# Optimization experiments

Hardware: AMD Instinct MI355X
Metric: run time of the kernel (lower is better)

The kernel has to match this reference:

```python
import jax, jax.numpy as jnp
import numpy as np

B, S, E = 8, 1025, 768
H, D = 12, 64  # num_heads, head_dim


def setup_inputs() -> dict:
    key = jax.random.key(0)
    ks = jax.random.split(key, 11)
    sc = 1.0 / np.sqrt(E)
    def lin(k):
        kw, kb = jax.random.split(k)
        return (jax.random.normal(kw, (E, E), jnp.float32) * sc,
                jax.random.normal(kb, (E,), jnp.float32) * sc)
    Wq, bq = lin(ks[0]); Wk, bk = lin(ks[1]); Wv, bv = lin(ks[2])
    Wc, bc = lin(ks[3]); Wo, bo = lin(ks[4])
    x = jax.random.normal(ks[5], (B, S, E), jnp.float32)
    return {"x": x, "Wq": Wq, "bq": bq, "Wk": Wk, "bk": bk,
            "Wv": Wv, "bv": bv, "Wc": Wc, "bc": bc, "Wo": Wo, "bo": bo}


def _heads(y, b, n):
    # [b, n, E] -> [b, H, n, D]
    return y.reshape(b, n, H, D).transpose(0, 2, 1, 3)


def reference(x, Wq, bq, Wk, bk, Wv, bv, Wc, bc, Wo, bo):
    b, s, e = x.shape
    n = s - 1  # special_cls strips the CLS token
    cls_token = x[:, 0, :]            # [b, E]
    xt = x[:, 1:, :]                  # [b, n, E]

    q = _heads(xt @ Wq.T + bq, b, n)  # [b, H, n, D]
    k = _heads(xt @ Wk.T + bk, b, n)
    v = _heads(xt @ Wv.T + bv, b, n)

    qk_dot = jnp.einsum('bhqd,bhkd->bhqk', q, k)             # [b,H,n,n]
    q_norm2 = jnp.clip((q ** 2).sum(-1, keepdims=True), 1e-5)  # [b,H,n,1]

    c = (cls_token @ Wc.T + bc).reshape(b, 1, H, D).transpose(0, 2, 1, 3)  # [b,H,1,D]
    cq_dot = jnp.einsum('bhod,bhqd->bhoq', c, q)             # [b,H,1,n]
    c_norm2 = jnp.clip((c ** 2).sum(-1, keepdims=True), 1e-5)  # [b,H,1,1]

    attn_logits = qk_dot * cq_dot.transpose(0, 1, 3, 2) / (q_norm2 * jnp.sqrt(D * c_norm2))

    ck_dot = jnp.einsum('bhod,bhkd->bhok', c, k)             # [b,H,1,n]
    attn_logits_for_cls = ck_dot / jnp.sqrt(D * c_norm2)
    cls_out = jnp.einsum('bhok,bhkd->bhod', attn_logits_for_cls, v).reshape(b, 1, H * D)

    attn = jax.nn.softmax(attn_logits, axis=-1)              # [b,H,n,n]
    values = jnp.einsum('bhqk,bhkd->bhqd', attn, v)          # [b,H,n,D]

    cls_out = (cls_token[:, None, :] + cls_out) * 0.5        # [b,1,E]
    values = jnp.concatenate(
        [cls_out, values.transpose(0, 2, 1, 3).reshape(b, n, e)], axis=1)  # [b,S,E]
    out = values @ Wo.T + bo
    return out, attn
```

## Files before the change

### kernel.cpp

```cpp
#include <hip/hip_runtime.h>

#define B_ 8
#define S_ 1025
#define E_ 768
#define H_ 12
#define D_ 64
#define N_ 1024
#define M_OUT (B_*S_)

typedef _Float16 half8_t __attribute__((ext_vector_type(8)));
typedef _Float16 half4_t __attribute__((ext_vector_type(4)));
typedef short short8_t __attribute__((ext_vector_type(8)));
typedef float f32x4 __attribute__((ext_vector_type(4)));

#define MFMA_F16(A, B, C)  __builtin_amdgcn_mfma_f32_16x16x32_f16((A), (B), (C), 0, 0, 0)
#define MFMA_BF16(A, B, C) __builtin_amdgcn_mfma_f32_16x16x32_bf16((A), (B), (C), 0, 0, 0)

__device__ __forceinline__ unsigned short f2bf(float f) {
  unsigned u = __float_as_uint(f);
  u += 0x7FFFu + ((u >> 16) & 1u);
  return (unsigned short)(u >> 16);
}
__device__ __forceinline__ float bf2f(unsigned short s) {
  return __uint_as_float(((unsigned)s) << 16);
}

__global__ __launch_bounds__(256) void split_x_kernel(
    const float* __restrict__ x, _Float16* __restrict__ xh, _Float16* __restrict__ xl)
{
  const int idx = blockIdx.x * 256 + threadIdx.x;
  const int row = idx / 192;
  const int c   = (idx % 192) * 4;
  const int xrow = row + (row >> 10) + 1;
  float4 v = *(const float4*)&x[(long)xrow*E_ + c];
  float f[4] = {v.x, v.y, v.z, v.w};
  half4_t hs, ls;
  #pragma unroll
  for (int t = 0; t < 4; ++t) {
    _Float16 hh = (_Float16)f[t];
    hs[t] = hh; ls[t] = (_Float16)(f[t] - (float)hh);
  }
  *(half4_t*)&xh[(long)row*E_ + c] = hs;
  *(half4_t*)&xl[(long)row*E_ + c] = ls;
}

__global__ __launch_bounds__(256) void split_w_kernel(
    const float* __restrict__ W0, const float* __restrict__ W1,
    const float* __restrict__ W2, const float* __restrict__ W3,
    _Float16* __restrict__ h0, _Float16* __restrict__ l0,
    _Float16* __restrict__ h1, _Float16* __restrict__ l1,
    _Float16* __restrict__ h2, _Float16* __restrict__ l2,
    _Float16* __restrict__ h3, _Float16* __restrict__ l3)
{
  const int which = blockIdx.y;
  const float* __restrict__ W = (which==0)?W0:(which==1)?W1:(which==2)?W2:W3;
  _Float16* __restrict__ oh   = (which==0)?h0:(which==1)?h1:(which==2)?h2:h3;
  _Float16* __restrict__ ol   = (which==0)?l0:(which==1)?l1:(which==2)?l2:l3;
  const int idx = blockIdx.x * 256 + threadIdx.x;
  const long off = (long)idx * 4;
  float4 v = *(const float4*)&W[off];
  float f[4] = {v.x, v.y, v.z, v.w};
  half4_t hs, ls;
  #pragma unroll
  for (int t = 0; t < 4; ++t) {
    _Float16 hh = (_Float16)f[t];
    hs[t] = hh; ls[t] = (_Float16)(f[t] - (float)hh);
  }
  *(half4_t*)&oh[off] = hs;
  *(half4_t*)&ol[off] = ls;
}

__global__ __launch_bounds__(256) void proj_qkv_kernel(
    const _Float16* __restrict__ xh, const _Float16* __restrict__ xl,
    const _Float16* __restrict__ wqh, const _Float16* __restrict__ wql,
    const _Float16* __restrict__ wkh, const _Float16* __restrict__ wkl,
    const _Float16* __restrict__ wvh, const _Float16* __restrict__ wvl,
    const float* __restrict__ bq, const float* __restrict__ bk, const float* __restrict__ bv,
    _Float16* __restrict__ qh, _Float16* __restrict__ ql,
    _Float16* __restrict__ kh, _Float16* __restrict__ kl,
    unsigned short* __restrict__ vth, unsigned short* __restrict__ vtl)
{
  __shared__ _Float16 Ah[128][40];
  __shared__ _Float16 Al[128][40];
  __shared__ _Float16 Bh[128][40];
  __shared__ _Float16 Bl[128][40];

  const int which = blockIdx.z;
  const _Float16* __restrict__ wh = (which==0)?wqh:(which==1)?wkh:wvh;
  const _Float16* __restrict__ wl = (which==0)?wql:(which==1)?wkl:wvl;
  const float* __restrict__ bias  = (which==0)?bq:(which==1)?bk:bv;

  const int tid  = threadIdx.x;
  const int lane = tid & 63;
  const int wv   = tid >> 6;
  const int wm   = wv >> 1, wn = wv & 1;
  const int m0   = blockIdx.y * 128;
  const int n0   = blockIdx.x * 128;

  const int srow = tid >> 1;
  const int scol = (tid & 1) << 4;

  const long arow = (long)(m0 + srow) * E_ + scol;
  const long brow = (long)(n0 + srow) * E_ + scol;

  f32x4 acc[4][4] = {};

  const int fr = lane & 15;
  const int kb = (lane >> 4) << 3;
  const int ar0 = wm * 64 + fr;
  const int br0 = wn * 64 + fr;

  for (int k0 = 0; k0 < E_; k0 += 32) {
    half8_t a_h0 = *(const half8_t*)&xh[arow + k0];
    half8_t a_h1 = *(const half8_t*)&xh[arow + k0 + 8];
    half8_t a_l0 = *(const half8_t*)&xl[arow + k0];
    half8_t a_l1 = *(const half8_t*)&xl[arow + k0 + 8];
    half8_t b_h0 = *(const half8_t*)&wh[brow + k0];
    half8_t b_h1 = *(const half8_t*)&wh[brow + k0 + 8];
    half8_t b_l0 = *(const half8_t*)&wl[brow + k0];
    half8_t b_l1 = *(const half8_t*)&wl[brow + k0 + 8];
    __syncthreads();
    *(half8_t*)&Ah[srow][scol]   = a_h0;  *(half8_t*)&Ah[srow][scol+8] = a_h1;
    *(half8_t*)&Al[srow][scol]   = a_l0;  *(half8_t*)&Al[srow][scol+8] = a_l1;
    *(half8_t*)&Bh[srow][scol]   = b_h0;  *(half8_t*)&Bh[srow][scol+8] = b_h1;
    *(half8_t*)&Bl[srow][scol]   = b_l0;  *(half8_t*)&Bl[srow][scol+8] = b_l1;
    __syncthreads();

    half8_t fah[4], fal[4], fbh[4], fbl[4];
    #pragma unroll
    for (int mi = 0; mi < 4; ++mi) {
      fah[mi] = *(const half8_t*)&Ah[ar0 + mi*16][kb];
      fal[mi] = *(const half8_t*)&Al[ar0 + mi*16][kb];
    }
    #pragma unroll
    for (int ni = 0; ni < 4; ++ni) {
      fbh[ni] = *(const half8_t*)&Bh[br0 + ni*16][kb];
      fbl[ni] = *(const half8_t*)&Bl[br0 + ni*16][kb];
    }
    #pragma unroll
    for (int mi = 0; mi < 4; ++mi)
      #pragma unroll
      for (int ni = 0; ni < 4; ++ni) {
        acc[mi][ni] = MFMA_F16(fah[mi], fbh[ni], acc[mi][ni]);
        acc[mi][ni] = MFMA_F16(fal[mi], fbh[ni], acc[mi][ni]);
        acc[mi][ni] = MFMA_F16(fah[mi], fbl[ni], acc[mi][ni]);
      }
  }

  const int rr = (lane >> 4) << 2;
  if (which < 2) {
    _Float16* __restrict__ oh = (which==0) ? qh : kh;
    _Float16* __restrict__ ol = (which==0) ? ql : kl;
    #pragma unroll
    for (int ni = 0; ni < 4; ++ni) {
      const int c = n0 + wn*64 + ni*16 + fr;
      const float bb = bias[c];
      #pragma unroll
      for (int mi = 0; mi < 4; ++mi) {
        const int row0 = m0 + wm*64 + mi*16 + rr;
        #pragma unroll
        for (int j = 0; j < 4; ++j) {
          float r = acc[mi][ni][j] + bb;
          _Float16 hh = (_Float16)r;
          oh[(long)(row0+j)*E_ + c] = hh;
          ol[(long)(row0+j)*E_ + c] = (_Float16)(r - (float)hh);
        }
      }
    }
  } else {
    #pragma unroll
    for (int ni = 0; ni < 4; ++ni) {
      const int c = n0 + wn*64 + ni*16 + fr;
      const int h_ = c >> 6, d_ = c & 63;
      const float bb = bias[c];
      #pragma unroll
      for (int mi = 0; mi < 4; ++mi) {
        const int row0 = m0 + wm*64 + mi*16 + rr;
        #pragma unroll
        for (int j = 0; j < 4; ++j) {
          const int row = row0 + j;
          const int b_ = row >> 10, n_ = row & 1023;
          float r = acc[mi][ni][j] + bb;
          unsigned short hb = f2bf(r);
          const long o = ((long)(b_*H_ + h_)*64 + d_)*N_ + n_;
          vth[o] = hb;
          vtl[o] = f2bf(r - bf2f(hb));
        }
      }
    }
  }
}

__global__ __launch_bounds__(256) void proj_out_kernel(
    const _Float16* __restrict__ ah_g, const _Float16* __restrict__ al_g,
    const _Float16* __restrict__ wh, const _Float16* __restrict__ wl,
    const float* __restrict__ bias, float* __restrict__ out)
{
  __shared__ _Float16 Ah[128][40];
  __shared__ _Float16 Al[128][40];
  __shared__ _Float16 Bh[128][40];
  __shared__ _Float16 Bl[128][40];

  const int tid  = threadIdx.x;
  const int lane = tid & 63;
  const int wv   = tid >> 6;
  const int wm   = wv >> 1, wn = wv & 1;
  const int m0   = blockIdx.y * 128;
  const int n0   = blockIdx.x * 128;

  const int srow = tid >> 1;
  const int scol = (tid & 1) << 4;

  const int gm = m0 + srow;
  const bool aok = gm < M_OUT;
  const long arow = (long)gm * E_ + scol;
  const long brow = (long)(n0 + srow) * E_ + scol;

  f32x4 acc[4][4] = {};

  const int fr = lane & 15;
  const int kb = (lane >> 4) << 3;
  const int ar0 = wm * 64 + fr;
  const int br0 = wn * 64 + fr;

  for (int k0 = 0; k0 < E_; k0 += 32) {
    half8_t a_h0 = {}, a_h1 = {}, a_l0 = {}, a_l1 = {};
    if (aok) {
      a_h0 = *(const half8_t*)&ah_g[arow + k0];
      a_h1 = *(const half8_t*)&ah_g[arow + k0 + 8];
      a_l0 = *(const half8_t*)&al_g[arow + k0];
      a_l1 = *(const half8_t*)&al_g[arow + k0 + 8];
    }
    half8_t b_h0 = *(const half8_t*)&wh[brow + k0];
    half8_t b_h1 = *(const half8_t*)&wh[brow + k0 + 8];
    half8_t b_l0 = *(const half8_t*)&wl[brow + k0];
    half8_t b_l1 = *(const half8_t*)&wl[brow + k0 + 8];
    __syncthreads();
    *(half8_t*)&Ah[srow][scol]   = a_h0;  *(half8_t*)&Ah[srow][scol+8] = a_h1;
    *(half8_t*)&Al[srow][scol]   = a_l0;  *(half8_t*)&Al[srow][scol+8] = a_l1;
    *(half8_t*)&Bh[srow][scol]   = b_h0;  *(half8_t*)&Bh[srow][scol+8] = b_h1;
    *(half8_t*)&Bl[srow][scol]   = b_l0;  *(half8_t*)&Bl[srow][scol+8] = b_l1;
    __syncthreads();

    half8_t fah[4], fal[4], fbh[4], fbl[4];
    #pragma unroll
    for (int mi = 0; mi < 4; ++mi) {
      fah[mi] = *(const half8_t*)&Ah[ar0 + mi*16][kb];
      fal[mi] = *(const half8_t*)&Al[ar0 + mi*16][kb];
    }
    #pragma unroll
    for (int ni = 0; ni < 4; ++ni) {
      fbh[ni] = *(const half8_t*)&Bh[br0 + ni*16][kb];
      fbl[ni] = *(const half8_t*)&Bl[br0 + ni*16][kb];
    }
    #pragma unroll
    for (int mi = 0; mi < 4; ++mi)
      #pragma unroll
      for (int ni = 0; ni < 4; ++ni) {
        acc[mi][ni] = MFMA_F16(fah[mi], fbh[ni], acc[mi][ni]);
        acc[mi][ni] = MFMA_F16(fal[mi], fbh[ni], acc[mi][ni]);
        acc[mi][ni] = MFMA_F16(fah[mi], fbl[ni], acc[mi][ni]);
      }
  }

  const int rr = (lane >> 4) << 2;
  #pragma unroll
  for (int ni = 0; ni < 4; ++ni) {
    const int c = n0 + wn*64 + ni*16 + fr;
    const float bb = bias[c];
    #pragma unroll
    for (int mi = 0; mi < 4; ++mi) {
      const int row = m0 + wm*64 + mi*16 + rr;
      #pragma unroll
      for (int j = 0; j < 4; ++j) {
        if (row + j < M_OUT)
          out[(long)(row + j) * E_ + c] = acc[mi][ni][j] + bb;
      }
    }
  }
}

__global__ __launch_bounds__(64) void cls_c_kernel(
    const float* __restrict__ x, const float* __restrict__ Wc, const float* __restrict__ bc,
    float* __restrict__ cbuf, float* __restrict__ cdenom)
{
  const int bh = blockIdx.x;
  const int b = bh / H_, h = bh % H_;
  const int d = threadIdx.x;
  const float* xr = x + (long)b*S_*E_;
  const float* wr = Wc + (long)(h*D_ + d)*E_;
  float acc = 0.f;
  for (int j = 0; j < E_; j += 4) {
    float4 xw = *(const float4*)&xr[j];
    float4 ww = *(const float4*)&wr[j];
    acc += xw.x*ww.x + xw.y*ww.y + xw.z*ww.z + xw.w*ww.w;
  }
  acc += bc[h*D_ + d];
  cbuf[bh*D_ + d] = acc;
  float sq = acc*acc;
  #pragma unroll
  for (int off = 32; off > 0; off >>= 1) sq += __shfl_xor(sq, off);
  if (d == 0) cdenom[bh] = rsqrtf((float)D_ * fmaxf(sq, 1e-5f));
}

__global__ __launch_bounds__(256) void attn_kernel(
    const _Float16* __restrict__ qh, const _Float16* __restrict__ ql,
    const _Float16* __restrict__ kh, const _Float16* __restrict__ kl,
    const unsigned short* __restrict__ vth, const unsigned short* __restrict__ vtl,
    const float* __restrict__ cbuf, const float* __restrict__ cdenom,
    _Float16* __restrict__ valsh, _Float16* __restrict__ vall,
    float* __restrict__ rowl_g, float* __restrict__ attn)
{
  __shared__ short QPh[64][72];
  __shared__ short QPl[64][72];
  __shared__ short Kh_s[64][72];
  __shared__ short Kl_s[64][72];
  __shared__ short Vth_s[64][72];
  __shared__ short Vtl_s[64][72];
  __shared__ float cs[64];
  __shared__ float rowscale_s[64];
  __shared__ float rowsum2[2][64];

  const int qt = blockIdx.x, h = blockIdx.y, b = blockIdx.z;
  const int bh = b * H_ + h;
  const int q0 = qt * 64;
  const int tid  = threadIdx.x;
  const int lane = tid & 63;
  const int wv   = tid >> 6;
  const int wm   = wv >> 1, wn = wv & 1;
  const int fr   = lane & 15;
  const int g    = lane >> 4;
  const int lr   = tid >> 2;
  const int lc   = (tid & 3) * 16;

  {
    const long qbase = ((long)b*N_ + q0 + lr)*E_ + h*D_ + lc;
    *(half8_t*)&QPh[lr][lc]   = *(const half8_t*)&qh[qbase];
    *(half8_t*)&QPh[lr][lc+8] = *(const half8_t*)&qh[qbase+8];
    *(half8_t*)&QPl[lr][lc]   = *(const half8_t*)&ql[qbase];
    *(half8_t*)&QPl[lr][lc+8] = *(const half8_t*)&ql[qbase+8];
  }
  if (tid < 64) cs[tid] = cbuf[bh*D_ + tid];
  const float cdn = cdenom[bh];
  __syncthreads();

  if (tid < 64) {
    const _Float16* qhr = (const _Float16*)QPh[tid];
    const _Float16* qlr = (const _Float16*)QPl[tid];
    float qn2 = 0.f, cq = 0.f;
    #pragma unroll 8
    for (int d = 0; d < 64; ++d) {
      float qv = (float)qhr[d] + (float)qlr[d];
      qn2 = fmaf(qv, qv, qn2);
      cq  = fmaf(cs[d], qv, cq);
    }
    rowscale_s[tid] = cq * cdn / fmaxf(qn2, 1e-5f);
  }

  half8_t qfh[2][2], qfl[2][2];
  #pragma unroll
  for (int mi = 0; mi < 2; ++mi)
    #pragma unroll
    for (int ks = 0; ks < 2; ++ks) {
      qfh[mi][ks] = *(const half8_t*)&QPh[wm*32 + mi*16 + fr][ks*32 + g*8];
      qfl[mi][ks] = *(const half8_t*)&QPl[wm*32 + mi*16 + fr][ks*32 + g*8];
    }
  __syncthreads();

  float rs[2][4];
  #pragma unroll
  for (int mi = 0; mi < 2; ++mi)
    #pragma unroll
    for (int j = 0; j < 4; ++j)
      rs[mi][j] = rowscale_s[wm*32 + mi*16 + g*4 + j];

  float psum[2][4] = {};
  f32x4 acc[2][2] = {};

  for (int kt = 0; kt < 16; ++kt) {
    __syncthreads();
    {
      const long kbase = ((long)b*N_ + kt*64 + lr)*E_ + h*D_ + lc;
      *(half8_t*)&Kh_s[lr][lc]   = *(const half8_t*)&kh[kbase];
      *(half8_t*)&Kh_s[lr][lc+8] = *(const half8_t*)&kh[kbase+8];
      *(half8_t*)&Kl_s[lr][lc]   = *(const half8_t*)&kl[kbase];
      *(half8_t*)&Kl_s[lr][lc+8] = *(const half8_t*)&kl[kbase+8];
    }
    {
      const long vbase = ((long)bh*64 + lr)*N_ + kt*64 + lc;
      *(short8_t*)&Vth_s[lr][lc]   = *(const short8_t*)(vth + vbase);
      *(short8_t*)&Vth_s[lr][lc+8] = *(const short8_t*)(vth + vbase + 8);
      *(short8_t*)&Vtl_s[lr][lc]   = *(const short8_t*)(vtl + vbase);
      *(short8_t*)&Vtl_s[lr][lc+8] = *(const short8_t*)(vtl + vbase + 8);
    }
    __syncthreads();

    f32x4 sacc[2][2] = {};
    #pragma unroll
    for (int ks = 0; ks < 2; ++ks) {
      half8_t kfh[2], kfl[2];
      #pragma unroll
      for (int ni = 0; ni < 2; ++ni) {
        kfh[ni] = *(const half8_t*)&Kh_s[wn*32 + ni*16 + fr][ks*32 + g*8];
        kfl[ni] = *(const half8_t*)&Kl_s[wn*32 + ni*16 + fr][ks*32 + g*8];
      }
      #pragma unroll
      for (int mi = 0; mi < 2; ++mi)
        #pragma unroll
        for (int ni = 0; ni < 2; ++ni) {
          sacc[mi][ni] = MFMA_F16(qfh[mi][ks], kfh[ni], sacc[mi][ni]);
          sacc[mi][ni] = MFMA_F16(qfl[mi][ks], kfh[ni], sacc[mi][ni]);
          sacc[mi][ni] = MFMA_F16(qfh[mi][ks], kfl[ni], sacc[mi][ni]);
        }
    }

    #pragma unroll
    for (int mi = 0; mi < 2; ++mi)
      #pragma unroll
      for (int ni = 0; ni < 2; ++ni)
        #pragma unroll
        for (int j = 0; j < 4; ++j) {
          const int row = wm*32 + mi*16 + g*4 + j;
          const int col = wn*32 + ni*16 + fr;
          float s = sacc[mi][ni][j] * rs[mi][j];
          float p = __expf(fminf(s, 60.f));
          psum[mi][j] += p;
          attn[((long)(bh*N_ + q0 + row) << 10) + kt*64 + col] = p;
          unsigned short hb = f2bf(p);
          QPh[row][col] = (short)hb;
          QPl[row][col] = (short)f2bf(p - bf2f(hb));
        }
    __syncthreads();

    #pragma unroll
    for (int ks = 0; ks < 2; ++ks) {
      short8_t pfh[2], pfl[2], vfh[2], vfl[2];
      #pragma unroll
      for (int mi = 0; mi < 2; ++mi) {
        pfh[mi] = *(const short8_t*)&QPh[wm*32 + mi*16 + fr][ks*32 + g*8];
        pfl[mi] = *(const short8_t*)&QPl[wm*32 + mi*16 + fr][ks*32 + g*8];
      }
      #pragma unroll
      for (int nj = 0; nj < 2; ++nj) {
        vfh[nj] = *(const short8_t*)&Vth_s[wn*32 + nj*16 + fr][ks*32 + g*8];
        vfl[nj] = *(const short8_t*)&Vtl_s[wn*32 + nj*16 + fr][ks*32 + g*8];
      }
      #pragma unroll
      for (int mi = 0; mi < 2; ++mi)
        #pragma unroll
        for (int nj = 0; nj < 2; ++nj) {
          acc[mi][nj] = MFMA_BF16(pfh[mi], vfh[nj], acc[mi][nj]);
          acc[mi][nj] = MFMA_BF16(pfl[mi], vfh[nj], acc[mi][nj]);
          acc[mi][nj] = MFMA_BF16(pfh[mi], vfl[nj], acc[mi][nj]);
        }
    }
  }

  #pragma unroll
  for (int mi = 0; mi < 2; ++mi)
    #pragma unroll
    for (int j = 0; j < 4; ++j) {
      float v = psum[mi][j];
      v += __shfl_xor(v, 1);
      v += __shfl_xor(v, 2);
      v += __shfl_xor(v, 4);
      v += __shfl_xor(v, 8);
      psum[mi][j] = v;
    }
  __syncthreads();
  if (fr == 0) {
    #pragma unroll
    for (int mi = 0; mi < 2; ++mi)
      #pragma unroll
      for (int j = 0; j < 4; ++j)
        rowsum2[wn][wm*32 + mi*16 + g*4 + j] = psum[mi][j];
  }
  __syncthreads();

  if (tid < 64)
    rowl_g[(long)bh*N_ + q0 + tid] = rowsum2[0][tid] + rowsum2[1][tid];

  #pragma unroll
  for (int mi = 0; mi < 2; ++mi)
    #pragma unroll
    for (int j = 0; j < 4; ++j) {
      const int row = wm*32 + mi*16 + g*4 + j;
      const float inv = 1.0f / (rowsum2[0][row] + rowsum2[1][row]);
      #pragma unroll
      for (int nj = 0; nj < 2; ++nj) {
        const int col = wn*32 + nj*16 + fr;
        const long vo = ((long)b*S_ + 1 + q0 + row)*E_ + h*D_ + col;
        float r = acc[mi][nj][j] * inv;
        _Float16 hh = (_Float16)r;
        valsh[vo] = hh;
        vall[vo]  = (_Float16)(r - (float)hh);
      }
    }
}

__global__ __launch_bounds__(256) void cls_attn_kernel(
    const float* __restrict__ x,
    const _Float16* __restrict__ kh, const _Float16* __restrict__ kl,
    const unsigned short* __restrict__ vth, const unsigned short* __restrict__ vtl,
    const float* __restrict__ cbuf, const float* __restrict__ cdenom,
    _Float16* __restrict__ valsh, _Float16* __restrict__ vall)
{
  __shared__ float cs[64];
  __shared__ float part[4][64];
  const int bh = blockIdx.x;
  const int b = bh / H_, h = bh % H_;
  const int tid = threadIdx.x;
  const int wv = tid >> 6, lane = tid & 63;
  if (tid < 64) cs[tid] = cbuf[bh*D_ + tid];
  __syncthreads();
  float acc = 0.f;
  const long kbase0 = (long)b*N_*E_ + h*D_ + lane;
  const long vtbase = ((long)bh*64 + lane)*N_;
  for (int kk = wv*256; kk < wv*256 + 256; ++kk) {
    const long kbase = kbase0 + (long)kk*E_;
    float kv = (float)kh[kbase] + (float)kl[kbase];
    float s = cs[lane] * kv;
    s += __shfl_xor(s, 1);  s += __shfl_xor(s, 2);  s += __shfl_xor(s, 4);
    s += __shfl_xor(s, 8);  s += __shfl_xor(s, 16); s += __shfl_xor(s, 32);
    float vvv = bf2f(vth[vtbase + kk]) + bf2f(vtl[vtbase + kk]);
    acc = fmaf(s, vvv, acc);
  }
  part[wv][lane] = acc;
  __syncthreads();
  if (tid < 64) {
    const float tot = (part[0][tid] + part[1][tid] + part[2][tid] + part[3][tid]) * cdenom[bh];
    const float cls = x[(long)b*S_*E_ + h*D_ + tid];
    float r = (cls + tot) * 0.5f;
    const long vo = (long)b*S_*E_ + h*D_ + tid;
    _Float16 hh = (_Float16)r;
    valsh[vo] = hh;
    vall[vo]  = (_Float16)(r - (float)hh);
  }
}

__global__ __launch_bounds__(256) void rescale_kernel(
    float* __restrict__ attn, const float* __restrict__ rowl_g)
{
  const long row = blockIdx.x;
  const float inv = 1.0f / rowl_g[row];
  float* p = attn + (row << 10) + threadIdx.x * 4;
  float4 u = *(float4*)p;
  u.x *= inv; u.y *= inv; u.z *= inv; u.w *= inv;
  *(float4*)p = u;
}

extern "C" void kernel_launch(void* const* d_in, const int* in_sizes, int n_in,
                              void* d_out, int out_size, void* d_ws, size_t ws_size,
                              hipStream_t stream) {
  (void)in_sizes; (void)n_in; (void)out_size; (void)ws_size;
  const float* x  = (const float*)d_in[0];
  const float* Wq = (const float*)d_in[1];
  const float* bq = (const float*)d_in[2];
  const float* Wk = (const float*)d_in[3];
  const float* bk = (const float*)d_in[4];
  const float* Wv = (const float*)d_in[5];
  const float* bv = (const float*)d_in[6];
  const float* Wc = (const float*)d_in[7];
  const float* bc = (const float*)d_in[8];
  const float* Wo = (const float*)d_in[9];
  const float* bo = (const float*)d_in[10];

  const long XSZ = (long)8192 * E_;
  const long WSZ = (long)E_ * E_;
  const long QSZ = (long)B_ * N_ * E_;
  const long VSZ = (long)B_ * S_ * E_;

  float* outp = (float*)d_out;
  float* attn = outp + VSZ;

  _Float16* xh  = (_Float16*)attn;
  _Float16* xl  = xh + XSZ;
  _Float16* wqh = xl + XSZ;
  _Float16* wql = wqh + WSZ;
  _Float16* wkh = wql + WSZ;
  _Float16* wkl = wkh + WSZ;
  _Float16* wvh = wkl + WSZ;
  _Float16* wvl = wvh + WSZ;

  _Float16* qh = (_Float16*)d_ws;
  _Float16* ql = qh + QSZ;
  _Float16* kh = ql + QSZ;
  _Float16* kl = kh + QSZ;
  unsigned short* vth = (unsigned short*)(kl + QSZ);
  unsigned short* vtl = vth + QSZ;
  _Float16* valsh = (_Float16*)(vtl + QSZ);
  _Float16* vall  = valsh + VSZ;
  _Float16* woh   = vall + VSZ;
  _Float16* wol   = woh + WSZ;
  float* cbuf = (float*)(wol + WSZ);
  float* cden = cbuf + B_*H_*D_;
  float* rowl = cden + B_*H_;

  split_x_kernel<<<6144, 256, 0, stream>>>(x, xh, xl);
  split_w_kernel<<<dim3(576, 4), 256, 0, stream>>>(Wq, Wk, Wv, Wo,
      wqh, wql, wkh, wkl, wvh, wvl, woh, wol);
  proj_qkv_kernel<<<dim3(6, 64, 3), 256, 0, stream>>>(xh, xl,
      wqh, wql, wkh, wkl, wvh, wvl, bq, bk, bv, qh, ql, kh, kl, vth, vtl);
  cls_c_kernel<<<B_*H_, 64, 0, stream>>>(x, Wc, bc, cbuf, cden);
  attn_kernel<<<dim3(16, H_, B_), 256, 0, stream>>>(qh, ql, kh, kl, vth, vtl,
      cbuf, cden, valsh, vall, rowl, attn);
  cls_attn_kernel<<<B_*H_, 256, 0, stream>>>(x, kh, kl, vth, vtl, cbuf, cden, valsh, vall);
  rescale_kernel<<<B_*H_*N_, 256, 0, stream>>>(attn, rowl);
  proj_out_kernel<<<dim3(6, 65), 256, 0, stream>>>(valsh, vall, woh, wol, bo, outp);
}
```

Baseline: 1.037 ms.

## Fuse attention normalization into a recompute pass and stage V transpose through LDS

The attention kernel no longer writes unnormalized probabilities and then rescales them in a separate kernel. After computing row sums, it recomputes QK^T over all key tiles and writes the normalized probabilities once, which removes a full read-modify-write pass over the large attn tensor and drops the rescale launch at the cost of extra MFMA and exp work. The V projection epilogue now transposes through swizzled shared memory so it can write vectorized, coalesced rows instead of scattered 2-byte stores. The values buffer is kept in fp32, and the fp16 hi/lo split moves into the output projection's load path.

```diff
diff --git a/kernel.cpp b/kernel.cpp
--- a/kernel.cpp
+++ b/kernel.cpp
@@ -80,10 +80,11 @@
     _Float16* __restrict__ kh, _Float16* __restrict__ kl,
     unsigned short* __restrict__ vth, unsigned short* __restrict__ vtl)
 {
-  __shared__ _Float16 Ah[128][40];
-  __shared__ _Float16 Al[128][40];
-  __shared__ _Float16 Bh[128][40];
-  __shared__ _Float16 Bl[128][40];
+  __shared__ __align__(16) unsigned char smem_raw[40960];
+  _Float16 (* const Ah)[40] = (_Float16 (*)[40])(smem_raw);
+  _Float16 (* const Al)[40] = (_Float16 (*)[40])(smem_raw + 10240);
+  _Float16 (* const Bh)[40] = (_Float16 (*)[40])(smem_raw + 20480);
+  _Float16 (* const Bl)[40] = (_Float16 (*)[40])(smem_raw + 30720);
 
   const int which = blockIdx.z;
   const _Float16* __restrict__ wh = (which==0)?wqh:(which==1)?wkh:wvh;
@@ -168,31 +169,44 @@
       }
     }
   } else {
-    #pragma unroll
-    for (int ni = 0; ni < 4; ++ni) {
-      const int c = n0 + wn*64 + ni*16 + fr;
-      const int h_ = c >> 6, d_ = c & 63;
-      const float bb = bias[c];
-      #pragma unroll
-      for (int mi = 0; mi < 4; ++mi) {
-        const int row0 = m0 + wm*64 + mi*16 + rr;
+    __syncthreads();
+    short (* const Vt)[136] = (short (*)[136])(smem_raw);
+    const int b_     = m0 >> 10;
+    const int n_base = m0 & 1023;
+    const int crow = tid >> 1, hf = tid & 1;
+    const int cg   = n0 + crow;
+    const long obase = ((long)(b_*H_ + (cg >> 6))*64 + (cg & 63))*N_ + n_base + hf*64;
+    const int rswz = (crow & 7) << 3;
+    #pragma unroll
+    for (int plane = 0; plane < 2; ++plane) {
+      #pragma unroll
+      for (int ni = 0; ni < 4; ++ni) {
+        const int cl = wn*64 + ni*16 + fr;
+        const float bb = bias[n0 + cl];
         #pragma unroll
-        for (int j = 0; j < 4; ++j) {
-          const int row = row0 + j;
-          const int b_ = row >> 10, n_ = row & 1023;
-          float r = acc[mi][ni][j] + bb;
-          unsigned short hb = f2bf(r);
-          const long o = ((long)(b_*H_ + h_)*64 + d_)*N_ + n_;
-          vth[o] = hb;
-          vtl[o] = f2bf(r - bf2f(hb));
-        }
-      }
+        for (int mi = 0; mi < 4; ++mi)
+          #pragma unroll
+          for (int j = 0; j < 4; ++j) {
+            const int rl = wm*64 + mi*16 + rr + j;
+            float r = acc[mi][ni][j] + bb;
+            unsigned short hb = f2bf(r);
+            unsigned short val = plane ? f2bf(r - bf2f(hb)) : hb;
+            Vt[cl][rl ^ ((cl & 7) << 3)] = (short)val;
+          }
+      }
+      __syncthreads();
+      unsigned short* __restrict__ dst = plane ? vtl : vth;
+      #pragma unroll
+      for (int t = 0; t < 8; ++t)
+        *(short8_t*)&dst[obase + t*8] =
+            *(const short8_t*)&Vt[crow][(hf*64 + t*8) ^ rswz];
+      __syncthreads();
     }
   }
 }
 
 __global__ __launch_bounds__(256) void proj_out_kernel(
-    const _Float16* __restrict__ ah_g, const _Float16* __restrict__ al_g,
+    const float* __restrict__ A,
     const _Float16* __restrict__ wh, const _Float16* __restrict__ wl,
     const float* __restrict__ bias, float* __restrict__ out)
 {
@@ -224,20 +238,31 @@
   const int br0 = wn * 64 + fr;
 
   for (int k0 = 0; k0 < E_; k0 += 32) {
-    half8_t a_h0 = {}, a_h1 = {}, a_l0 = {}, a_l1 = {};
+    float4 a0 = make_float4(0.f,0.f,0.f,0.f), a1 = a0, a2 = a0, a3 = a0;
     if (aok) {
-      a_h0 = *(const half8_t*)&ah_g[arow + k0];
-      a_h1 = *(const half8_t*)&ah_g[arow + k0 + 8];
-      a_l0 = *(const half8_t*)&al_g[arow + k0];
-      a_l1 = *(const half8_t*)&al_g[arow + k0 + 8];
+      a0 = *(const float4*)&A[arow + k0];
+      a1 = *(const float4*)&A[arow + k0 + 4];
+      a2 = *(const float4*)&A[arow + k0 + 8];
+      a3 = *(const float4*)&A[arow + k0 + 12];
     }
     half8_t b_h0 = *(const half8_t*)&wh[brow + k0];
     half8_t b_h1 = *(const half8_t*)&wh[brow + k0 + 8];
     half8_t b_l0 = *(const half8_t*)&wl[brow + k0];
     half8_t b_l1 = *(const half8_t*)&wl[brow + k0 + 8];
     __syncthreads();
-    *(half8_t*)&Ah[srow][scol]   = a_h0;  *(half8_t*)&Ah[srow][scol+8] = a_h1;
-    *(half8_t*)&Al[srow][scol]   = a_l0;  *(half8_t*)&Al[srow][scol+8] = a_l1;
+    {
+      float av[16] = {a0.x,a0.y,a0.z,a0.w,a1.x,a1.y,a1.z,a1.w,
+                      a2.x,a2.y,a2.z,a2.w,a3.x,a3.y,a3.z,a3.w};
+      half8_t ah0, ah1, alo0, alo1;
+      #pragma unroll
+      for (int t = 0; t < 8; ++t) {
+        _Float16 hh;
+        hh = (_Float16)av[t];   ah0[t] = hh; alo0[t] = (_Float16)(av[t]   - (float)hh);
+        hh = (_Float16)av[t+8]; ah1[t] = hh; alo1[t] = (_Float16)(av[t+8] - (float)hh);
+      }
+      *(half8_t*)&Ah[srow][scol]   = ah0;  *(half8_t*)&Ah[srow][scol+8] = ah1;
+      *(half8_t*)&Al[srow][scol]   = alo0; *(half8_t*)&Al[srow][scol+8] = alo1;
+    }
     *(half8_t*)&Bh[srow][scol]   = b_h0;  *(half8_t*)&Bh[srow][scol+8] = b_h1;
     *(half8_t*)&Bl[srow][scol]   = b_l0;  *(half8_t*)&Bl[srow][scol+8] = b_l1;
     __syncthreads();
@@ -308,8 +333,7 @@
     const _Float16* __restrict__ kh, const _Float16* __restrict__ kl,
     const unsigned short* __restrict__ vth, const unsigned short* __restrict__ vtl,
     const float* __restrict__ cbuf, const float* __restrict__ cdenom,
-    _Float16* __restrict__ valsh, _Float16* __restrict__ vall,
-    float* __restrict__ rowl_g, float* __restrict__ attn)
+    float* __restrict__ vals, float* __restrict__ attn)
 {
   __shared__ short QPh[64][72];
   __shared__ short QPl[64][72];
@@ -425,7 +449,6 @@
           float s = sacc[mi][ni][j] * rs[mi][j];
           float p = __expf(fminf(s, 60.f));
           psum[mi][j] += p;
-          attn[((long)(bh*N_ + q0 + row) << 10) + kt*64 + col] = p;
           unsigned short hb = f2bf(p);
           QPh[row][col] = (short)hb;
           QPl[row][col] = (short)f2bf(p - bf2f(hb));
@@ -477,25 +500,70 @@
   }
   __syncthreads();
 
-  if (tid < 64)
-    rowl_g[(long)bh*N_ + q0 + tid] = rowsum2[0][tid] + rowsum2[1][tid];
-
+  float invr[2][4];
   #pragma unroll
   for (int mi = 0; mi < 2; ++mi)
     #pragma unroll
     for (int j = 0; j < 4; ++j) {
       const int row = wm*32 + mi*16 + g*4 + j;
-      const float inv = 1.0f / (rowsum2[0][row] + rowsum2[1][row]);
+      invr[mi][j] = 1.0f / (rowsum2[0][row] + rowsum2[1][row]);
+    }
+
+  #pragma unroll
+  for (int mi = 0; mi < 2; ++mi)
+    #pragma unroll
+    for (int j = 0; j < 4; ++j) {
+      const int row = wm*32 + mi*16 + g*4 + j;
       #pragma unroll
       for (int nj = 0; nj < 2; ++nj) {
         const int col = wn*32 + nj*16 + fr;
-        const long vo = ((long)b*S_ + 1 + q0 + row)*E_ + h*D_ + col;
-        float r = acc[mi][nj][j] * inv;
-        _Float16 hh = (_Float16)r;
-        valsh[vo] = hh;
-        vall[vo]  = (_Float16)(r - (float)hh);
-      }
-    }
+        vals[((long)b*S_ + 1 + q0 + row)*E_ + h*D_ + col] = acc[mi][nj][j] * invr[mi][j];
+      }
+    }
+
+  for (int kt = 0; kt < 16; ++kt) {
+    __syncthreads();
+    {
+      const long kbase = ((long)b*N_ + kt*64 + lr)*E_ + h*D_ + lc;
+      *(half8_t*)&Kh_s[lr][lc]   = *(const half8_t*)&kh[kbase];
+      *(half8_t*)&Kh_s[lr][lc+8] = *(const half8_t*)&kh[kbase+8];
+      *(half8_t*)&Kl_s[lr][lc]   = *(const half8_t*)&kl[kbase];
+      *(half8_t*)&Kl_s[lr][lc+8] = *(const half8_t*)&kl[kbase+8];
+    }
+    __syncthreads();
+
+    f32x4 sacc[2][2] = {};
+    #pragma unroll
+    for (int ks = 0; ks < 2; ++ks) {
+      half8_t kfh[2], kfl[2];
+      #pragma unroll
+      for (int ni = 0; ni < 2; ++ni) {
+        kfh[ni] = *(const half8_t*)&Kh_s[wn*32 + ni*16 + fr][ks*32 + g*8];
+        kfl[ni] = *(const half8_t*)&Kl_s[wn*32 + ni*16 + fr][ks*32 + g*8];
+      }
+      #pragma unroll
+      for (int mi = 0; mi < 2; ++mi)
+        #pragma unroll
+        for (int ni = 0; ni < 2; ++ni) {
+          sacc[mi][ni] = MFMA_F16(qfh[mi][ks], kfh[ni], sacc[mi][ni]);
+          sacc[mi][ni] = MFMA_F16(qfl[mi][ks], kfh[ni], sacc[mi][ni]);
+          sacc[mi][ni] = MFMA_F16(qfh[mi][ks], kfl[ni], sacc[mi][ni]);
+        }
+    }
+
+    #pragma unroll
+    for (int mi = 0; mi < 2; ++mi)
+      #pragma unroll
+      for (int ni = 0; ni < 2; ++ni)
+        #pragma unroll
+        for (int j = 0; j < 4; ++j) {
+          const int row = wm*32 + mi*16 + g*4 + j;
+          const int col = wn*32 + ni*16 + fr;
+          float s = sacc[mi][ni][j] * rs[mi][j];
+          float p = __expf(fminf(s, 60.f));
+          attn[((long)(bh*N_ + q0 + row) << 10) + kt*64 + col] = p * invr[mi][j];
+        }
+  }
 }
 
 __global__ __launch_bounds__(256) void cls_attn_kernel(
@@ -503,7 +571,7 @@
     const _Float16* __restrict__ kh, const _Float16* __restrict__ kl,
     const unsigned short* __restrict__ vth, const unsigned short* __restrict__ vtl,
     const float* __restrict__ cbuf, const float* __restrict__ cdenom,
-    _Float16* __restrict__ valsh, _Float16* __restrict__ vall)
+    float* __restrict__ vals)
 {
   __shared__ float cs[64];
   __shared__ float part[4][64];
@@ -530,23 +598,8 @@
   if (tid < 64) {
     const float tot = (part[0][tid] + part[1][tid] + part[2][tid] + part[3][tid]) * cdenom[bh];
     const float cls = x[(long)b*S_*E_ + h*D_ + tid];
-    float r = (cls + tot) * 0.5f;
-    const long vo = (long)b*S_*E_ + h*D_ + tid;
-    _Float16 hh = (_Float16)r;
-    valsh[vo] = hh;
-    vall[vo]  = (_Float16)(r - (float)hh);
-  }
-}
-
-__global__ __launch_bounds__(256) void rescale_kernel(
-    float* __restrict__ attn, const float* __restrict__ rowl_g)
-{
-  const long row = blockIdx.x;
-  const float inv = 1.0f / rowl_g[row];
-  float* p = attn + (row << 10) + threadIdx.x * 4;
-  float4 u = *(float4*)p;
-  u.x *= inv; u.y *= inv; u.z *= inv; u.w *= inv;
-  *(float4*)p = u;
+    vals[(long)b*S_*E_ + h*D_ + tid] = (cls + tot) * 0.5f;
+  }
 }
 
 extern "C" void kernel_launch(void* const* d_in, const int* in_sizes, int n_in,
@@ -588,13 +641,11 @@
   _Float16* kl = kh + QSZ;
   unsigned short* vth = (unsigned short*)(kl + QSZ);
   unsigned short* vtl = vth + QSZ;
-  _Float16* valsh = (_Float16*)(vtl + QSZ);
-  _Float16* vall  = valsh + VSZ;
-  _Float16* woh   = vall + VSZ;
-  _Float16* wol   = woh + WSZ;
+  float* vals = (float*)(vtl + QSZ);
+  _Float16* woh = (_Float16*)(vals + VSZ);
+  _Float16* wol = woh + WSZ;
   float* cbuf = (float*)(wol + WSZ);
   float* cden = cbuf + B_*H_*D_;
-  float* rowl = cden + B_*H_;
 
   split_x_kernel<<<6144, 256, 0, stream>>>(x, xh, xl);
   split_w_kernel<<<dim3(576, 4), 256, 0, stream>>>(Wq, Wk, Wv, Wo,
@@ -603,8 +654,7 @@
       wqh, wql, wkh, wkl, wvh, wvl, bq, bk, bv, qh, ql, kh, kl, vth, vtl);
   cls_c_kernel<<<B_*H_, 64, 0, stream>>>(x, Wc, bc, cbuf, cden);
   attn_kernel<<<dim3(16, H_, B_), 256, 0, stream>>>(qh, ql, kh, kl, vth, vtl,
-      cbuf, cden, valsh, vall, rowl, attn);
-  cls_attn_kernel<<<B_*H_, 256, 0, stream>>>(x, kh, kl, vth, vtl, cbuf, cden, valsh, vall);
-  rescale_kernel<<<B_*H_*N_, 256, 0, stream>>>(attn, rowl);
-  proj_out_kernel<<<dim3(6, 65), 256, 0, stream>>>(valsh, vall, woh, wol, bo, outp);
-}
+      cbuf, cden, vals, attn);
+  cls_attn_kernel<<<B_*H_, 256, 0, stream>>>(x, kh, kl, vth, vtl, cbuf, cden, vals);
+  proj_out_kernel<<<dim3(6, 65), 256, 0, stream>>>(vals, woh, wol, bo, outp);
+}
```

Measured after the change: 935.0 us. 1.11x faster.
